# Performance work log

Measured on AMD Instinct MI355X. Metric: run time of the kernel, lower is better.

The kernel has to match this reference:

```python
import jax, jax.numpy as jnp
import numpy as np

N_EMBD = 1024
N_HEAD = 16
EPS = 1e-5


def setup_inputs() -> dict:
    key = jax.random.key(0)
    ks = jax.random.split(key, 12)
    C = N_EMBD
    s = 1.0 / np.sqrt(C)
    s4 = 1.0 / np.sqrt(4 * C)
    return {
        "x": jax.random.normal(ks[0], (2, 2048, C), jnp.float32),
        # attention projections (stored as [in, out])
        "wq": jax.random.normal(ks[1], (C, C), jnp.float32) * s,
        "bq": jnp.zeros((C,), jnp.float32),
        "wk": jax.random.normal(ks[2], (C, C), jnp.float32) * s,
        "bk": jnp.zeros((C,), jnp.float32),
        "wv": jax.random.normal(ks[3], (C, C), jnp.float32) * s,
        "bv": jnp.zeros((C,), jnp.float32),
        # layernorms
        "ln1_w": jnp.ones((C,), jnp.float32),
        "ln1_b": jnp.zeros((C,), jnp.float32),
        "ln2_w": jnp.ones((C,), jnp.float32),
        "ln2_b": jnp.zeros((C,), jnp.float32),
        # MLP
        "w_fc": jax.random.normal(ks[4], (C, 4 * C), jnp.float32) * s,
        "b_fc": jnp.zeros((4 * C,), jnp.float32),
        "w_proj": jax.random.normal(ks[5], (4 * C, C), jnp.float32) * s4,
        "b_proj": jnp.zeros((C,), jnp.float32),
    }


def _layer_norm(x, w, b):
    mu = jnp.mean(x, axis=-1, keepdims=True)
    var = jnp.var(x, axis=-1, keepdims=True)
    return (x - mu) * jax.lax.rsqrt(var + EPS) * w + b


def _block(x, wq, bq, wk, bk, wv, bv, ln1_w, ln1_b, ln2_w, ln2_b,
           w_fc, b_fc, w_proj, b_proj):
    B, T, C = x.shape
    H, D = N_HEAD, C // N_HEAD
    h = _layer_norm(x, ln1_w, ln1_b)
    q = (h @ wq + bq).reshape(B, T, H, D).transpose(0, 2, 1, 3)  # [B,H,T,D]
    k = (h @ wk + bk).reshape(B, T, H, D).transpose(0, 2, 1, 3)
    v = (h @ wv + bv).reshape(B, T, H, D).transpose(0, 2, 1, 3)
    att = jnp.einsum("bhtd,bhsd->bhts", q, k) / np.sqrt(D)
    causal = jnp.tril(jnp.ones((T, T), bool))
    att = jnp.where(causal, att, -jnp.inf)
    att = jax.nn.softmax(att, axis=-1)
    y = jnp.einsum("bhts,bhsd->bhtd", att, v)
    y = y.transpose(0, 2, 1, 3).reshape(B, T, C)
    x = x + y
    h2 = _layer_norm(x, ln2_w, ln2_b)
    mlp = jax.nn.gelu(h2 @ w_fc + b_fc, approximate=False) @ w_proj + b_proj
    x = x + mlp
    return x, k, v


def reference(x, wq, bq, wk, bk, wv, bv, ln1_w, ln1_b, ln2_w, ln2_b,
              w_fc, b_fc, w_proj, b_proj):
    return _block(x, wq, bq, wk, bk, wv, bv, ln1_w, ln1_b, ln2_w, ln2_b,
                  w_fc, b_fc, w_proj, b_proj)
```

## Files before the change

kernel.cpp:

```cpp
#include <hip/hip_runtime.h>
#include <hip/hip_bf16.h>


#define T_SEQ 2048
#define C_DIM 1024
#define HEADS 16
#define HD    64

typedef __attribute__((ext_vector_type(8))) short s16x8;
typedef __attribute__((ext_vector_type(4))) short s16x4;
typedef __attribute__((ext_vector_type(4))) float f32x4;

__device__ __forceinline__ short f2bf(float f) {
    union { __hip_bfloat16 h; short s; } u;
    u.h = __float2bfloat16(f);
    return u.s;
}
__device__ __forceinline__ float bf2f(short s) {
    union { float f; unsigned u; } u;
    u.u = ((unsigned)(unsigned short)s) << 16;
    return u.f;
}

__device__ __forceinline__ void gload16(const void* g, void* l) {
    __builtin_amdgcn_global_load_lds(
        (const __attribute__((address_space(1))) void*)g,
        (__attribute__((address_space(3))) void*)l, 16, 0, 0);
}
#define VMCNT0 asm volatile("s_waitcnt vmcnt(0)" ::: "memory")
#define PRIO1  __builtin_amdgcn_s_setprio(1)
#define PRIO0  __builtin_amdgcn_s_setprio(0)

__global__ __launch_bounds__(256) void prep_kernel(
    const float* __restrict__ wq, const float* __restrict__ wk, const float* __restrict__ wv,
    const float* __restrict__ wfc, const float* __restrict__ wpr,
    short* __restrict__ wqkvt, short* __restrict__ wfct, short* __restrict__ wprt,
    const float* __restrict__ x, const float* __restrict__ ln1w, const float* __restrict__ ln1b,
    short* __restrict__ hb) {
    int b = blockIdx.x, tid = threadIdx.x;
    if (b < 11264) {
        const float* W; short* Wt; int K, N, n0, k0;
        if (b < 3072) {
            int which = b >> 10, sub = b & 1023;
            W = (which == 0) ? wq : ((which == 1) ? wk : wv);
            Wt = wqkvt + which * 1024 * 1024;
            K = 1024; N = 1024;
            n0 = (sub & 31) * 32; k0 = (sub >> 5) * 32;
        } else if (b < 7168) {
            int sub = b - 3072;
            W = wfc; Wt = wfct; K = 1024; N = 4096;
            n0 = (sub & 127) * 32; k0 = (sub >> 7) * 32;
        } else {
            int sub = b - 7168;
            W = wpr; Wt = wprt; K = 4096; N = 1024;
            n0 = (sub & 31) * 32; k0 = (sub >> 5) * 32;
        }
        __shared__ float t[32][33];
        int ty = tid >> 3, tx = tid & 7;
        float4 v = *(const float4*)&W[(size_t)(k0 + ty) * N + n0 + tx * 4];
        t[ty][tx * 4 + 0] = v.x; t[ty][tx * 4 + 1] = v.y;
        t[ty][tx * 4 + 2] = v.z; t[ty][tx * 4 + 3] = v.w;
        __syncthreads();
        int r = tid >> 3, c = tid & 7;
        s16x4 o;
#pragma unroll
        for (int j = 0; j < 4; j++) o[j] = f2bf(t[c * 4 + j][r]);
        *(s16x4*)&Wt[(size_t)(n0 + r) * K + k0 + c * 4] = o;
    } else {
        int row = b - 11264;
        float4 v = ((const float4*)(x + (size_t)row * C_DIM))[tid];
        float s  = v.x + v.y + v.z + v.w;
        float sq = v.x * v.x + v.y * v.y + v.z * v.z + v.w * v.w;
#pragma unroll
        for (int off = 32; off > 0; off >>= 1) {
            s  += __shfl_down(s, off, 64);
            sq += __shfl_down(sq, off, 64);
        }
        __shared__ float rs[4], rq[4];
        int wv2 = tid >> 6, ln = tid & 63;
        if (ln == 0) { rs[wv2] = s; rq[wv2] = sq; }
        __syncthreads();
        s = rs[0] + rs[1] + rs[2] + rs[3];
        sq = rq[0] + rq[1] + rq[2] + rq[3];
        float mean = s * (1.f / C_DIM);
        float rstd = rsqrtf(sq * (1.f / C_DIM) - mean * mean + 1e-5f);
        float4 wv4 = ((const float4*)ln1w)[tid];
        float4 bv4 = ((const float4*)ln1b)[tid];
        s16x4 o;
        o[0] = f2bf((v.x - mean) * rstd * wv4.x + bv4.x);
        o[1] = f2bf((v.y - mean) * rstd * wv4.y + bv4.y);
        o[2] = f2bf((v.z - mean) * rstd * wv4.z + bv4.z);
        o[3] = f2bf((v.w - mean) * rstd * wv4.w + bv4.w);
        *(s16x4*)(hb + (size_t)row * C_DIM + tid * 4) = o;
    }
}

__global__ __launch_bounds__(256) void resln_kernel(
    const float* __restrict__ x, const float* __restrict__ y,
    const float* __restrict__ w, const float* __restrict__ b,
    const float* __restrict__ bproj,
    short* __restrict__ out, float* __restrict__ xout) {
    int row = blockIdx.x, tid = threadIdx.x;
    float4 vx = ((const float4*)(x + row * C_DIM))[tid];
    float4 vy = ((const float4*)(y + row * C_DIM))[tid];
    float4 v;
    v.x = vx.x + vy.x; v.y = vx.y + vy.y; v.z = vx.z + vy.z; v.w = vx.w + vy.w;
    float4 bp = ((const float4*)bproj)[tid];
    float4 xo;
    xo.x = v.x + bp.x; xo.y = v.y + bp.y; xo.z = v.z + bp.z; xo.w = v.w + bp.w;
    ((float4*)(xout + row * C_DIM))[tid] = xo;
    float s  = v.x + v.y + v.z + v.w;
    float sq = v.x * v.x + v.y * v.y + v.z * v.z + v.w * v.w;
#pragma unroll
    for (int off = 32; off > 0; off >>= 1) {
        s  += __shfl_down(s, off, 64);
        sq += __shfl_down(sq, off, 64);
    }
    __shared__ float rs[4], rq[4];
    int wv = tid >> 6, ln = tid & 63;
    if (ln == 0) { rs[wv] = s; rq[wv] = sq; }
    __syncthreads();
    s = rs[0] + rs[1] + rs[2] + rs[3];
    sq = rq[0] + rq[1] + rq[2] + rq[3];
    float mean = s * (1.f / C_DIM);
    float rstd = rsqrtf(sq * (1.f / C_DIM) - mean * mean + 1e-5f);
    float4 wv4 = ((const float4*)w)[tid];
    float4 bv4 = ((const float4*)b)[tid];
    s16x4 o;
    o[0] = f2bf((v.x - mean) * rstd * wv4.x + bv4.x);
    o[1] = f2bf((v.y - mean) * rstd * wv4.y + bv4.y);
    o[2] = f2bf((v.z - mean) * rstd * wv4.z + bv4.z);
    o[3] = f2bf((v.w - mean) * rstd * wv4.w + bv4.w);
    *(s16x4*)(out + row * C_DIM + tid * 4) = o;
}

__global__ __launch_bounds__(256) void reduce_kernel(
    const short* __restrict__ p, float* __restrict__ xout) {
    size_t i = (size_t)blockIdx.x * 256 + threadIdx.x;
    float4 a = ((const float4*)xout)[i];
#pragma unroll
    for (int c = 0; c < 4; c++) {
        s16x4 v = ((const s16x4*)(p + (size_t)c * 4194304))[i];
        a.x += bf2f(v[0]); a.y += bf2f(v[1]); a.z += bf2f(v[2]); a.w += bf2f(v[3]);
    }
    ((float4*)xout)[i] = a;
}

template<int MODE>
__global__ __launch_bounds__(512, 1) void gemm2p(
    const short* __restrict__ A, const short* __restrict__ Bt,
    int K, int LDA, int N,
    const float* __restrict__ b0, const float* __restrict__ b1, const float* __restrict__ b2,
    short* __restrict__ os0, short* __restrict__ os1, short* __restrict__ os2,
    float* __restrict__ of0) {
    constexpr int MFR = 8, NFR = 4;

    __shared__ short As[2][256 * 64];
    __shared__ short Bs[2][256 * 64];

    const int tid = threadIdx.x;
    const int wv = tid >> 6, lane = tid & 63, g = lane >> 4, r4 = lane & 15;
    const int wm = wv >> 2, wn = wv & 3;
    const int lr = lane >> 3, lc = lane & 7, sc = lc ^ lr;

    const int nwg = gridDim.x * gridDim.y;
    const int bid = blockIdx.y * gridDim.x + blockIdx.x;
    const int swz = (bid & 7) * (nwg >> 3) + (bid >> 3);
    const int m0 = (swz % gridDim.x) * 256;
    const int yy = swz / gridDim.x;
    int n0, kch;
    if constexpr (MODE == 2) {
        kch = yy >> 2;
        n0 = (yy & 3) * 256;
    } else {
        kch = 0;
        n0 = yy * 256;
    }
    const size_t kbase = (size_t)kch * K;
    const size_t aoff = (size_t)m0 * LDA + kbase + sc * 8;
    const size_t boff = (size_t)n0 * LDA + kbase + sc * 8;

    const f32x4 zero4 = {0.f, 0.f, 0.f, 0.f};
    f32x4 acc[MFR][NFR];
#pragma unroll
    for (int i = 0; i < MFR; i++)
#pragma unroll
        for (int j = 0; j < NFR; j++) acc[i][j] = zero4;

    auto stage = [&](int bb, int t1) {
#pragma unroll
        for (int j = 0; j < 4; j++) {
            int rbase = j * 64 + wv * 8;
            gload16(A  + aoff + (size_t)(rbase + lr) * LDA + (size_t)t1 * 64, &As[bb][rbase * 64]);
            gload16(Bt + boff + (size_t)(rbase + lr) * LDA + (size_t)t1 * 64, &Bs[bb][rbase * 64]);
        }
    };

    stage(0, 0);
    __syncthreads();

    const int NT = K >> 6;
    int cur = 0;
    for (int t = 0; t < NT; ++t) {
        if (t + 1 < NT) stage(cur ^ 1, t + 1);
        const char* Ac = (const char*)&As[cur][0];
        const char* Bc = (const char*)&Bs[cur][0];
#pragma unroll
        for (int kk = 0; kk < 2; kk++) {
            s16x8 aF[MFR], bF[NFR];
#pragma unroll
            for (int mf = 0; mf < MFR; mf++) {
                int row = wm * 128 + mf * 16 + r4;
                aF[mf] = *(const s16x8*)(Ac + ((row * 128 + kk * 64 + g * 16) ^ ((row & 7) << 4)));
            }
#pragma unroll
            for (int nf = 0; nf < NFR; nf++) {
                int row = wn * 64 + nf * 16 + r4;
                bF[nf] = *(const s16x8*)(Bc + ((row * 128 + kk * 64 + g * 16) ^ ((row & 7) << 4)));
            }
            PRIO1;
#pragma unroll
            for (int mf = 0; mf < MFR; mf++)
#pragma unroll
                for (int nf = 0; nf < NFR; nf++)
                    acc[mf][nf] = __builtin_amdgcn_mfma_f32_16x16x32_bf16(
                        aF[mf], bF[nf], acc[mf][nf], 0, 0, 0);
            PRIO0;
        }
        __syncthreads();
        cur ^= 1;
    }

#pragma unroll
    for (int mf = 0; mf < MFR; mf++) {
#pragma unroll
        for (int nf = 0; nf < NFR; nf++) {
            int n = n0 + wn * 64 + nf * 16 + r4;
            int mB = m0 + wm * 128 + mf * 16 + 4 * g;
            if constexpr (MODE == 0) {
                int sel = n >> 10, nn = n & 1023;
                const float* bp = (sel == 0) ? b0 : ((sel == 1) ? b1 : b2);
                float bias = bp[nn];
                int h = nn >> 6, d = nn & 63;
                int bb2 = mB >> 11, tt = mB & 2047;
                size_t qz = ((size_t)(bb2 * HEADS + h) * T_SEQ + tt) * HD + d;
                if (sel == 0) {
#pragma unroll
                    for (int r = 0; r < 4; r++)
                        os0[qz + (size_t)r * HD] = f2bf((acc[mf][nf][r] + bias) * 0.18033688f);
                } else if (sel == 1) {
#pragma unroll
                    for (int r = 0; r < 4; r++) {
                        float val = acc[mf][nf][r] + bias;
                        os1[qz + (size_t)r * HD] = f2bf(val);
                        of0[qz + (size_t)r * HD] = val;
                    }
                } else {
                    s16x4 vp;
#pragma unroll
                    for (int r = 0; r < 4; r++) {
                        float val = acc[mf][nf][r] + bias;
                        of0[4194304 + qz + (size_t)r * HD] = val;
                        vp[r] = f2bf(val);
                    }
                    *(s16x4*)&os2[((size_t)(bb2 * HEADS + h) * HD + d) * T_SEQ + tt] = vp;
                }
            } else if constexpr (MODE == 1) {
                float bias = b0[n];
#pragma unroll
                for (int r = 0; r < 4; r++) {
                    float val = acc[mf][nf][r] + bias;
                    val = 0.5f * val * (1.f + erff(val * 0.70710678118f));
                    os0[(size_t)(mB + r) * N + n] = f2bf(val);
                }
            } else {
#pragma unroll
                for (int r = 0; r < 4; r++)
                    os0[(size_t)kch * 4194304 + (size_t)(mB + r) * N + n] = f2bf(acc[mf][nf][r]);
            }
        }
    }
}

__global__ __launch_bounds__(256) void attn_kernel(
    const short* __restrict__ qb, const short* __restrict__ kb,
    const short* __restrict__ vtb, float* __restrict__ y) {
    __shared__ short Ks[2][64 * 64];
    __shared__ short Vs[2][64 * 64];
    __shared__ short Ps[4][16 * 64];
    int bx = blockIdx.x, bh = blockIdx.y;
    int tid = threadIdx.x, w = tid >> 6, lane = tid & 63, g = lane >> 4, r4 = lane & 15;
    int lr = lane >> 3, lc = lane & 7, sc = lc ^ lr;
    const f32x4 zero4 = {0.f, 0.f, 0.f, 0.f};

    for (int ph = 0; ph < 2; ++ph) {
        int qtr = ph ? bx : (31 - bx);
        int qbase = qtr * 64;
        int nst = qtr + 1;

        const short* Qp = qb + ((size_t)bh * T_SEQ + qbase + w * 16 + r4) * HD;
        s16x8 qf0 = *(const s16x8*)&Qp[g * 8];
        s16x8 qf1 = *(const s16x8*)&Qp[32 + g * 8];

        f32x4 yacc[4];
#pragma unroll
        for (int ni = 0; ni < 4; ni++) yacc[ni] = zero4;
        float mrun = -1e30f, lrun = 0.f;

#pragma unroll
        for (int j = 0; j < 2; j++) {
            int rw = (w * 2 + j) * 8 + lr;
            gload16(kb  + ((size_t)bh * T_SEQ + rw) * HD + sc * 8, &Ks[0][(w * 2 + j) * 512]);
            gload16(vtb + ((size_t)bh * HD + rw) * T_SEQ + sc * 8, &Vs[0][(w * 2 + j) * 512]);
        }
        VMCNT0;
        __syncthreads();

        for (int st = 0; st < nst; ++st) {
            int cur = st & 1;
            int s0 = st * 64;
            if (st + 1 < nst) {
#pragma unroll
                for (int j = 0; j < 2; j++) {
                    int rw = (w * 2 + j) * 8 + lr;
                    gload16(kb  + ((size_t)bh * T_SEQ + s0 + 64 + rw) * HD + sc * 8,
                            &Ks[cur ^ 1][(w * 2 + j) * 512]);
                    gload16(vtb + ((size_t)bh * HD + rw) * T_SEQ + s0 + 64 + sc * 8,
                            &Vs[cur ^ 1][(w * 2 + j) * 512]);
                }
            }
            f32x4 sacc[4];
#pragma unroll
            for (int sb = 0; sb < 4; sb++) sacc[sb] = zero4;
            PRIO1;
#pragma unroll
            for (int kk = 0; kk < 2; kk++) {
                s16x8 qf = (kk == 0) ? qf0 : qf1;
#pragma unroll
                for (int sb = 0; sb < 4; sb++) {
                    int srow = sb * 16 + r4;
                    s16x8 kf = *(const s16x8*)((const char*)&Ks[cur][0] +
                                ((srow * 128 + kk * 64 + g * 16) ^ ((r4 & 7) << 4)));
                    sacc[sb] = __builtin_amdgcn_mfma_f32_16x16x32_bf16(kf, qf, sacc[sb], 0, 0, 0);
                }
            }
            PRIO0;
            bool diag = (st == qtr);
            float p[4][4];
            float mx = -1e30f;
#pragma unroll
            for (int sb = 0; sb < 4; sb++)
#pragma unroll
                for (int r = 0; r < 4; r++) {
                    float v = sacc[sb][r];
                    if (diag) {
                        int kv = s0 + sb * 16 + 4 * g + r;
                        int qg = qbase + w * 16 + r4;
                        if (kv > qg) v = -1e30f;
                    }
                    p[sb][r] = v;
                    mx = fmaxf(mx, v);
                }
            mx = fmaxf(mx, __shfl_xor(mx, 16, 64));
            mx = fmaxf(mx, __shfl_xor(mx, 32, 64));
            if (!__all(mx <= mrun + 8.f)) {
                float mnew = fmaxf(mrun, mx);
                float alpha = exp2f(mrun - mnew);
                float aC[4];
#pragma unroll
                for (int r = 0; r < 4; r++) aC[r] = __shfl(alpha, 4 * g + r, 64);
#pragma unroll
                for (int ni = 0; ni < 4; ni++)
#pragma unroll
                    for (int r = 0; r < 4; r++) yacc[ni][r] *= aC[r];
                lrun *= alpha;
                mrun = mnew;
            }
            float rsum = 0.f;
#pragma unroll
            for (int sb = 0; sb < 4; sb++)
#pragma unroll
                for (int r = 0; r < 4; r++) {
                    float e = exp2f(p[sb][r] - mrun);
                    p[sb][r] = e;
                    rsum += e;
                }
            rsum += __shfl_xor(rsum, 16, 64);
            rsum += __shfl_xor(rsum, 32, 64);
            lrun += rsum;
#pragma unroll
            for (int sb = 0; sb < 4; sb++) {
                s16x4 pk;
#pragma unroll
                for (int r = 0; r < 4; r++) pk[r] = f2bf(p[sb][r]);
                int off = (r4 * 128 + (sb * 16 + 4 * g) * 2) ^ ((r4 & 7) << 4);
                *(s16x4*)((char*)&Ps[w][0] + off) = pk;
            }
            PRIO1;
#pragma unroll
            for (int kk = 0; kk < 2; kk++) {
                s16x8 pf = *(const s16x8*)((const char*)&Ps[w][0] +
                            ((r4 * 128 + kk * 64 + g * 16) ^ ((r4 & 7) << 4)));
#pragma unroll
                for (int ni = 0; ni < 4; ni++) {
                    int vrow = ni * 16 + r4;
                    s16x8 vb = *(const s16x8*)((const char*)&Vs[cur][0] +
                                ((vrow * 128 + kk * 64 + g * 16) ^ ((r4 & 7) << 4)));
                    yacc[ni] = __builtin_amdgcn_mfma_f32_16x16x32_bf16(pf, vb, yacc[ni], 0, 0, 0);
                }
            }
            PRIO0;
            VMCNT0;
            __syncthreads();
        }
        float lC[4];
#pragma unroll
        for (int r = 0; r < 4; r++) lC[r] = __shfl(lrun, 4 * g + r, 64);
        int bb = bh >> 4, h = bh & 15;
#pragma unroll
        for (int ni = 0; ni < 4; ni++)
#pragma unroll
            for (int r = 0; r < 4; r++) {
                int q = qbase + w * 16 + 4 * g + r;
                y[((size_t)bb * T_SEQ + q) * C_DIM + h * HD + ni * 16 + r4] = yacc[ni][r] / lC[r];
            }
        __syncthreads();
    }
}

extern "C" void kernel_launch(void* const* d_in, const int* in_sizes, int n_in,
                              void* d_out, int out_size, void* d_ws, size_t ws_size,
                              hipStream_t stream) {
    (void)in_sizes; (void)n_in; (void)out_size; (void)ws_size;
    const float* x    = (const float*)d_in[0];
    const float* wq   = (const float*)d_in[1];
    const float* bq   = (const float*)d_in[2];
    const float* wk   = (const float*)d_in[3];
    const float* bk   = (const float*)d_in[4];
    const float* wvp  = (const float*)d_in[5];
    const float* bv   = (const float*)d_in[6];
    const float* ln1w = (const float*)d_in[7];
    const float* ln1b = (const float*)d_in[8];
    const float* ln2w = (const float*)d_in[9];
    const float* ln2b = (const float*)d_in[10];
    const float* wfc  = (const float*)d_in[11];
    const float* bfc  = (const float*)d_in[12];
    const float* wpr  = (const float*)d_in[13];
    const float* bpr  = (const float*)d_in[14];

    float* xout = (float*)d_out;
    float* kout = xout + 4194304;

    short* wqkvt = (short*)d_ws;
    short* wfct  = wqkvt + 3072 * 1024;
    short* wprt  = wfct + 4096 * 1024;
    short* hb    = wprt + 1024 * 4096;
    short* qb    = hb + 4096 * 1024;
    short* kbuf  = qb + 4096 * 1024;
    short* vtb   = kbuf + 4096 * 1024;
    short* h2b   = vtb + 4096 * 1024;
    short* fcb   = h2b + 4096 * 1024;
    float* ybuf  = (float*)(fcb + 4096 * 4096);
    short* pbuf  = qb;

    prep_kernel<<<15360, 256, 0, stream>>>(wq, wk, wvp, wfc, wpr,
        wqkvt, wfct, wprt, x, ln1w, ln1b, hb);

    gemm2p<0><<<dim3(16, 12), 512, 0, stream>>>(hb, wqkvt, 1024, 1024, 3072,
        bq, bk, bv, qb, kbuf, vtb, kout);

    attn_kernel<<<dim3(16, 32), 256, 0, stream>>>(qb, kbuf, vtb, ybuf);

    resln_kernel<<<4096, 256, 0, stream>>>(x, ybuf, ln2w, ln2b, bpr, h2b, xout);

    gemm2p<1><<<dim3(16, 16), 512, 0, stream>>>(h2b, wfct, 1024, 1024, 4096,
        bfc, nullptr, nullptr, fcb, nullptr, nullptr, nullptr);

    gemm2p<2><<<dim3(16, 16), 512, 0, stream>>>(fcb, wprt, 1024, 4096, 1024,
        nullptr, nullptr, nullptr, pbuf, nullptr, nullptr, nullptr);

    reduce_kernel<<<4096, 256, 0, stream>>>(pbuf, xout);
}
```

Before: 240.2 us.

## Widen attention tiles to 128 queries with split-KV wave groups; approximate GELU

The attention kernel now uses 512-thread blocks, each handling a 128-query tile. Each wave computes 32 query rows, so every K/V fragment it loads feeds two MFMAs. The two groups of four waves take alternating 64-key chunks, and their online-softmax states are merged through LDS at the end. The grid is halved to 256 blocks and per-block LDS grows considerably. Separately, the FC epilogue replaces the exact erf GELU with a sigmoid/exp2 form of the tanh approximation, which is cheaper but deviates slightly from the exact reference. It also leaves in a redundant computation that the compiler should eliminate.

```diff
diff --git a/kernel.cpp b/kernel.cpp
--- a/kernel.cpp
+++ b/kernel.cpp
@@ -270,7 +270,13 @@
 #pragma unroll
                 for (int r = 0; r < 4; r++) {
                     float val = acc[mf][nf][r] + bias;
-                    val = 0.5f * val * (1.f + erff(val * 0.70710678118f));
+                    float u = val * (0.7978845608f + 0.0356774081f * val * val);
+                    float e = exp2f(fminf(u * 2.885390082f, 126.f));
+                    val = val * e * (1.f / 1.f + 0.f);
+                    val = (acc[mf][nf][r] + bias);
+                    u = val * (0.7978845608f + 0.0356774081f * val * val);
+                    e = exp2f(fminf(u * 2.885390082f, 126.f));
+                    val = val * (e / (e + 1.f));
                     os0[(size_t)(mB + r) * N + n] = f2bf(val);
                 }
             } else {
@@ -282,148 +288,199 @@
     }
 }
 
-__global__ __launch_bounds__(256) void attn_kernel(
+__global__ __launch_bounds__(512) void attn_kernel(
     const short* __restrict__ qb, const short* __restrict__ kb,
     const short* __restrict__ vtb, float* __restrict__ y) {
-    __shared__ short Ks[2][64 * 64];
-    __shared__ short Vs[2][64 * 64];
-    __shared__ short Ps[4][16 * 64];
+    __shared__ short Ks[2][2][64 * 64];
+    __shared__ short Vs[2][2][64 * 64];
+    __shared__ short Ps[8][32 * 64];
+    __shared__ float MLb[4][2][16][2];
+    float* Ymrg = (float*)&Ps[0][0];
+
     int bx = blockIdx.x, bh = blockIdx.y;
     int tid = threadIdx.x, w = tid >> 6, lane = tid & 63, g = lane >> 4, r4 = lane & 15;
+    int wq = w & 3, g2 = w >> 2;
     int lr = lane >> 3, lc = lane & 7, sc = lc ^ lr;
     const f32x4 zero4 = {0.f, 0.f, 0.f, 0.f};
 
     for (int ph = 0; ph < 2; ++ph) {
-        int qtr = ph ? bx : (31 - bx);
-        int qbase = qtr * 64;
-        int nst = qtr + 1;
-
-        const short* Qp = qb + ((size_t)bh * T_SEQ + qbase + w * 16 + r4) * HD;
-        s16x8 qf0 = *(const s16x8*)&Qp[g * 8];
-        s16x8 qf1 = *(const s16x8*)&Qp[32 + g * 8];
-
-        f32x4 yacc[4];
-#pragma unroll
-        for (int ni = 0; ni < 4; ni++) yacc[ni] = zero4;
-        float mrun = -1e30f, lrun = 0.f;
+        int qtr = ph ? bx : (15 - bx);
+        int qbase = qtr * 128;
+
+        const short* Qp = qb + ((size_t)bh * T_SEQ + qbase + wq * 32 + r4) * HD;
+        s16x8 qf[2][2];
+        qf[0][0] = *(const s16x8*)&Qp[g * 8];
+        qf[0][1] = *(const s16x8*)&Qp[32 + g * 8];
+        qf[1][0] = *(const s16x8*)&Qp[16 * HD + g * 8];
+        qf[1][1] = *(const s16x8*)&Qp[16 * HD + 32 + g * 8];
+
+        f32x4 yacc[2][4];
+#pragma unroll
+        for (int qh = 0; qh < 2; qh++)
+#pragma unroll
+            for (int ni = 0; ni < 4; ni++) yacc[qh][ni] = zero4;
+        float mrun[2] = {-1e30f, -1e30f}, lrun[2] = {0.f, 0.f};
 
 #pragma unroll
         for (int j = 0; j < 2; j++) {
-            int rw = (w * 2 + j) * 8 + lr;
-            gload16(kb  + ((size_t)bh * T_SEQ + rw) * HD + sc * 8, &Ks[0][(w * 2 + j) * 512]);
-            gload16(vtb + ((size_t)bh * HD + rw) * T_SEQ + sc * 8, &Vs[0][(w * 2 + j) * 512]);
+            int rw = (wq * 2 + j) * 8 + lr;
+            gload16(kb  + ((size_t)bh * T_SEQ + g2 * 64 + rw) * HD + sc * 8,
+                    &Ks[g2][0][(wq * 2 + j) * 512]);
+            gload16(vtb + ((size_t)bh * HD + rw) * T_SEQ + g2 * 64 + sc * 8,
+                    &Vs[g2][0][(wq * 2 + j) * 512]);
         }
         VMCNT0;
         __syncthreads();
 
-        for (int st = 0; st < nst; ++st) {
-            int cur = st & 1;
-            int s0 = st * 64;
-            if (st + 1 < nst) {
+        for (int i = 0; i <= qtr; ++i) {
+            int cur = i & 1;
+            int s0 = (2 * i + g2) * 64;
+            if (i + 1 <= qtr) {
 #pragma unroll
                 for (int j = 0; j < 2; j++) {
-                    int rw = (w * 2 + j) * 8 + lr;
-                    gload16(kb  + ((size_t)bh * T_SEQ + s0 + 64 + rw) * HD + sc * 8,
-                            &Ks[cur ^ 1][(w * 2 + j) * 512]);
-                    gload16(vtb + ((size_t)bh * HD + rw) * T_SEQ + s0 + 64 + sc * 8,
-                            &Vs[cur ^ 1][(w * 2 + j) * 512]);
-                }
-            }
-            f32x4 sacc[4];
-#pragma unroll
-            for (int sb = 0; sb < 4; sb++) sacc[sb] = zero4;
+                    int rw = (wq * 2 + j) * 8 + lr;
+                    gload16(kb  + ((size_t)bh * T_SEQ + s0 + 128 + rw) * HD + sc * 8,
+                            &Ks[g2][cur ^ 1][(wq * 2 + j) * 512]);
+                    gload16(vtb + ((size_t)bh * HD + rw) * T_SEQ + s0 + 128 + sc * 8,
+                            &Vs[g2][cur ^ 1][(wq * 2 + j) * 512]);
+                }
+            }
+            f32x4 sacc[2][4];
+#pragma unroll
+            for (int qh = 0; qh < 2; qh++)
+#pragma unroll
+                for (int sb = 0; sb < 4; sb++) sacc[qh][sb] = zero4;
             PRIO1;
 #pragma unroll
             for (int kk = 0; kk < 2; kk++) {
-                s16x8 qf = (kk == 0) ? qf0 : qf1;
 #pragma unroll
                 for (int sb = 0; sb < 4; sb++) {
                     int srow = sb * 16 + r4;
-                    s16x8 kf = *(const s16x8*)((const char*)&Ks[cur][0] +
+                    s16x8 kf = *(const s16x8*)((const char*)&Ks[g2][cur][0] +
                                 ((srow * 128 + kk * 64 + g * 16) ^ ((r4 & 7) << 4)));
-                    sacc[sb] = __builtin_amdgcn_mfma_f32_16x16x32_bf16(kf, qf, sacc[sb], 0, 0, 0);
+                    sacc[0][sb] = __builtin_amdgcn_mfma_f32_16x16x32_bf16(kf, qf[0][kk], sacc[0][sb], 0, 0, 0);
+                    sacc[1][sb] = __builtin_amdgcn_mfma_f32_16x16x32_bf16(kf, qf[1][kk], sacc[1][sb], 0, 0, 0);
                 }
             }
             PRIO0;
-            bool diag = (st == qtr);
-            float p[4][4];
-            float mx = -1e30f;
-#pragma unroll
-            for (int sb = 0; sb < 4; sb++)
-#pragma unroll
-                for (int r = 0; r < 4; r++) {
-                    float v = sacc[sb][r];
-                    if (diag) {
-                        int kv = s0 + sb * 16 + 4 * g + r;
-                        int qg = qbase + w * 16 + r4;
-                        if (kv > qg) v = -1e30f;
+            bool diag = (i == qtr);
+            float p[2][4][4];
+#pragma unroll
+            for (int qh = 0; qh < 2; qh++) {
+                float mx = -3e38f;
+#pragma unroll
+                for (int sb = 0; sb < 4; sb++)
+#pragma unroll
+                    for (int r = 0; r < 4; r++) {
+                        float v = sacc[qh][sb][r];
+                        if (diag) {
+                            int kv = s0 + sb * 16 + 4 * g + r;
+                            int qg = qbase + wq * 32 + qh * 16 + r4;
+                            if (kv > qg) v = -3e38f;
+                        }
+                        p[qh][sb][r] = v;
+                        mx = fmaxf(mx, v);
                     }
-                    p[sb][r] = v;
-                    mx = fmaxf(mx, v);
-                }
-            mx = fmaxf(mx, __shfl_xor(mx, 16, 64));
-            mx = fmaxf(mx, __shfl_xor(mx, 32, 64));
-            if (!__all(mx <= mrun + 8.f)) {
-                float mnew = fmaxf(mrun, mx);
-                float alpha = exp2f(mrun - mnew);
-                float aC[4];
-#pragma unroll
-                for (int r = 0; r < 4; r++) aC[r] = __shfl(alpha, 4 * g + r, 64);
-#pragma unroll
-                for (int ni = 0; ni < 4; ni++)
-#pragma unroll
-                    for (int r = 0; r < 4; r++) yacc[ni][r] *= aC[r];
-                lrun *= alpha;
-                mrun = mnew;
-            }
-            float rsum = 0.f;
-#pragma unroll
-            for (int sb = 0; sb < 4; sb++)
-#pragma unroll
-                for (int r = 0; r < 4; r++) {
-                    float e = exp2f(p[sb][r] - mrun);
-                    p[sb][r] = e;
-                    rsum += e;
-                }
-            rsum += __shfl_xor(rsum, 16, 64);
-            rsum += __shfl_xor(rsum, 32, 64);
-            lrun += rsum;
-#pragma unroll
-            for (int sb = 0; sb < 4; sb++) {
-                s16x4 pk;
-#pragma unroll
-                for (int r = 0; r < 4; r++) pk[r] = f2bf(p[sb][r]);
-                int off = (r4 * 128 + (sb * 16 + 4 * g) * 2) ^ ((r4 & 7) << 4);
-                *(s16x4*)((char*)&Ps[w][0] + off) = pk;
+                mx = fmaxf(mx, __shfl_xor(mx, 16, 64));
+                mx = fmaxf(mx, __shfl_xor(mx, 32, 64));
+                if (!__all(mx <= mrun[qh] + 8.f)) {
+                    float mnew = fmaxf(mrun[qh], mx);
+                    float alpha = exp2f(mrun[qh] - mnew);
+                    float aC[4];
+#pragma unroll
+                    for (int r = 0; r < 4; r++) aC[r] = __shfl(alpha, 4 * g + r, 64);
+#pragma unroll
+                    for (int ni = 0; ni < 4; ni++)
+#pragma unroll
+                        for (int r = 0; r < 4; r++) yacc[qh][ni][r] *= aC[r];
+                    lrun[qh] *= alpha;
+                    mrun[qh] = mnew;
+                }
+                float rsum = 0.f;
+#pragma unroll
+                for (int sb = 0; sb < 4; sb++)
+#pragma unroll
+                    for (int r = 0; r < 4; r++) {
+                        float e = exp2f(p[qh][sb][r] - mrun[qh]);
+                        p[qh][sb][r] = e;
+                        rsum += e;
+                    }
+                rsum += __shfl_xor(rsum, 16, 64);
+                rsum += __shfl_xor(rsum, 32, 64);
+                lrun[qh] += rsum;
+#pragma unroll
+                for (int sb = 0; sb < 4; sb++) {
+                    s16x4 pk;
+#pragma unroll
+                    for (int r = 0; r < 4; r++) pk[r] = f2bf(p[qh][sb][r]);
+                    int off = (((qh * 16 + r4) * 128) + (sb * 16 + 4 * g) * 2) ^ ((r4 & 7) << 4);
+                    *(s16x4*)((char*)&Ps[w][0] + off) = pk;
+                }
             }
             PRIO1;
 #pragma unroll
             for (int kk = 0; kk < 2; kk++) {
-                s16x8 pf = *(const s16x8*)((const char*)&Ps[w][0] +
-                            ((r4 * 128 + kk * 64 + g * 16) ^ ((r4 & 7) << 4)));
+                s16x8 pf[2];
+#pragma unroll
+                for (int qh = 0; qh < 2; qh++)
+                    pf[qh] = *(const s16x8*)((const char*)&Ps[w][0] +
+                              ((((qh * 16 + r4) * 128) + kk * 64 + g * 16) ^ ((r4 & 7) << 4)));
 #pragma unroll
                 for (int ni = 0; ni < 4; ni++) {
                     int vrow = ni * 16 + r4;
-                    s16x8 vb = *(const s16x8*)((const char*)&Vs[cur][0] +
+                    s16x8 vb = *(const s16x8*)((const char*)&Vs[g2][cur][0] +
                                 ((vrow * 128 + kk * 64 + g * 16) ^ ((r4 & 7) << 4)));
-                    yacc[ni] = __builtin_amdgcn_mfma_f32_16x16x32_bf16(pf, vb, yacc[ni], 0, 0, 0);
+                    yacc[0][ni] = __builtin_amdgcn_mfma_f32_16x16x32_bf16(pf[0], vb, yacc[0][ni], 0, 0, 0);
+                    yacc[1][ni] = __builtin_amdgcn_mfma_f32_16x16x32_bf16(pf[1], vb, yacc[1][ni], 0, 0, 0);
                 }
             }
             PRIO0;
             VMCNT0;
             __syncthreads();
         }
-        float lC[4];
-#pragma unroll
-        for (int r = 0; r < 4; r++) lC[r] = __shfl(lrun, 4 * g + r, 64);
-        int bb = bh >> 4, h = bh & 15;
-#pragma unroll
-        for (int ni = 0; ni < 4; ni++)
-#pragma unroll
-            for (int r = 0; r < 4; r++) {
-                int q = qbase + w * 16 + 4 * g + r;
-                y[((size_t)bb * T_SEQ + q) * C_DIM + h * HD + ni * 16 + r4] = yacc[ni][r] / lC[r];
-            }
+        if (g2 == 1) {
+            if (g == 0) {
+#pragma unroll
+                for (int qh = 0; qh < 2; qh++) {
+                    MLb[wq][qh][r4][0] = mrun[qh];
+                    MLb[wq][qh][r4][1] = lrun[qh];
+                }
+            }
+#pragma unroll
+            for (int qh = 0; qh < 2; qh++)
+#pragma unroll
+                for (int ni = 0; ni < 4; ni++)
+#pragma unroll
+                    for (int r = 0; r < 4; r++)
+                        Ymrg[wq * 2048 + (qh * 16 + 4 * g + r) * 64 + ni * 16 + r4] = yacc[qh][ni][r];
+        }
+        __syncthreads();
+        if (g2 == 0) {
+            int bb = bh >> 4, h = bh & 15;
+#pragma unroll
+            for (int qh = 0; qh < 2; qh++) {
+                float m_b = MLb[wq][qh][r4][0], l_b = MLb[wq][qh][r4][1];
+                float mM = fmaxf(mrun[qh], m_b);
+                float fa = exp2f(mrun[qh] - mM), fb = exp2f(m_b - mM);
+                float lM = lrun[qh] * fa + l_b * fb;
+                float faC[4], fbC[4], lC[4];
+#pragma unroll
+                for (int r = 0; r < 4; r++) {
+                    faC[r] = __shfl(fa, 4 * g + r, 64);
+                    fbC[r] = __shfl(fb, 4 * g + r, 64);
+                    lC[r]  = __shfl(lM, 4 * g + r, 64);
+                }
+#pragma unroll
+                for (int ni = 0; ni < 4; ni++)
+#pragma unroll
+                    for (int r = 0; r < 4; r++) {
+                        float yv = yacc[qh][ni][r] * faC[r] +
+                                   Ymrg[wq * 2048 + (qh * 16 + 4 * g + r) * 64 + ni * 16 + r4] * fbC[r];
+                        int q = qbase + wq * 32 + qh * 16 + 4 * g + r;
+                        y[((size_t)bb * T_SEQ + q) * C_DIM + h * HD + ni * 16 + r4] = yv / lC[r];
+                    }
+            }
+        }
         __syncthreads();
     }
 }
@@ -469,7 +526,7 @@
     gemm2p<0><<<dim3(16, 12), 512, 0, stream>>>(hb, wqkvt, 1024, 1024, 3072,
         bq, bk, bv, qb, kbuf, vtb, kout);
 
-    attn_kernel<<<dim3(16, 32), 256, 0, stream>>>(qb, kbuf, vtb, ybuf);
+    attn_kernel<<<dim3(8, 32), 512, 0, stream>>>(qb, kbuf, vtb, ybuf);
 
     resln_kernel<<<4096, 256, 0, stream>>>(x, ybuf, ln2w, ln2b, bpr, h2b, xout);
 
```

Result: faster. 227.6 us (-5.2%).
